# Performance work log

Measured on AMD Instinct MI355X. Metric: run time of the kernel, lower is better.

## Reference

```python
import jax, jax.numpy as jnp
import numpy as np

N = 100000
E = 1600000
IN_FEATS = 128
OUT_FEATS = 64


def setup_inputs() -> dict:
    key = jax.random.key(0)
    ks = jax.random.split(key, 8)
    node_feat = jax.random.normal(ks[0], (N, IN_FEATS), dtype=jnp.float32)
    edge_feat = jax.random.normal(ks[1], (E, 1), dtype=jnp.float32)
    # Linear params (PyTorch Linear: y = x @ W^T + b; we store W already transposed as [in, out])
    W_node = jax.random.normal(ks[2], (IN_FEATS, OUT_FEATS), dtype=jnp.float32) / np.sqrt(IN_FEATS)
    b_node = jax.random.normal(ks[3], (OUT_FEATS,), dtype=jnp.float32) * 0.01
    W_edge = jax.random.normal(ks[4], (1, OUT_FEATS), dtype=jnp.float32)
    b_edge = jax.random.normal(ks[5], (OUT_FEATS,), dtype=jnp.float32) * 0.01
    src = jax.random.randint(ks[6], (E,), 0, N, dtype=jnp.int32)
    dst = jax.random.randint(ks[7], (E,), 0, N, dtype=jnp.int32)
    return {"node_feat": node_feat, "edge_feat": edge_feat, "W_node": W_node,
            "b_node": b_node, "W_edge": W_edge, "b_edge": b_edge,
            "src": src, "dst": dst}


def reference(node_feat, edge_feat, W_node, b_node, W_edge, b_edge, src, dst):
    n_nodes = node_feat.shape[0]
    # node linear: h = node_fc(node_feat)  -> [N, out]
    h = node_feat @ W_node + b_node
    # edge linear: he = edge_fc(edge_feat) -> [E, out]
    he = edge_feat @ W_edge + b_edge
    # u_add_e: m = h[src] + he  (gather + add)  -> [E, out]
    m = h[src] + he
    # mean aggregate over destination nodes (segment mean; 0 for isolated nodes, as in DGL)
    msg_sum = jax.ops.segment_sum(m, dst, num_segments=n_nodes)  # [N, out]
    deg = jax.ops.segment_sum(jnp.ones((dst.shape[0],), dtype=m.dtype), dst, num_segments=n_nodes)  # [N]
    h_new = msg_sum / jnp.maximum(deg, 1.0)[:, None]
    return h_new
```

## Files before the change

### kernel.cpp

```cpp
#include <hip/hip_runtime.h>

#define IN_F 128
#define OUT_F 64
#define BSH 7
#define BNODES 128
#define NBMAX 800
#define MSC 6144
#define CAPB 4096

typedef __attribute__((ext_vector_type(8))) short short8;
typedef __attribute__((ext_vector_type(4))) float f32x4;

static __device__ __forceinline__ unsigned short f2bf(float f) {
    unsigned u = __float_as_uint(f);
    u += 0x7FFF + ((u >> 16) & 1);
    return (unsigned short)(u >> 16);
}

__global__ void prep_w(const float* __restrict__ W, unsigned short* __restrict__ Wt) {
    int i = blockIdx.x * 256 + threadIdx.x;
    if (i < OUT_F * IN_F) {
        int o = i >> 7, k = i & 127;
        Wt[i] = f2bf(W[k * OUT_F + o]);
    }
}

__global__ __launch_bounds__(256) void node_linear_mfma(const float* __restrict__ nf,
                                                        const unsigned short* __restrict__ Wt,
                                                        const float* __restrict__ bn,
                                                        unsigned short* __restrict__ h16,
                                                        int n_nodes, int n_tiles) {
    const int lane = threadIdx.x & 63;
    const int wid  = threadIdx.x >> 6;
    const int l15  = lane & 15;
    const int kq   = lane >> 4;

    short8 bfrag[4][4];
#pragma unroll
    for (int c = 0; c < 4; ++c)
#pragma unroll
        for (int ks = 0; ks < 4; ++ks)
            bfrag[c][ks] = *(const short8*)&Wt[(c * 16 + l15) * IN_F + ks * 32 + kq * 8];

    float bv[4];
#pragma unroll
    for (int c = 0; c < 4; ++c) bv[c] = bn[c * 16 + l15];

    for (int tile = blockIdx.x * 4 + wid; tile < n_tiles; tile += gridDim.x * 4) {
        int arow = tile * 16 + l15;
        if (arow >= n_nodes) arow = n_nodes - 1;
        const float* rp = nf + (size_t)arow * IN_F + kq * 8;

        f32x4 acc[4];
#pragma unroll
        for (int c = 0; c < 4; ++c) acc[c] = (f32x4){bv[c], bv[c], bv[c], bv[c]};

#pragma unroll
        for (int ks = 0; ks < 4; ++ks) {
            float4 x0 = *(const float4*)(rp + ks * 32);
            float4 x1 = *(const float4*)(rp + ks * 32 + 4);
            short8 af;
            af[0] = (short)f2bf(x0.x); af[1] = (short)f2bf(x0.y);
            af[2] = (short)f2bf(x0.z); af[3] = (short)f2bf(x0.w);
            af[4] = (short)f2bf(x1.x); af[5] = (short)f2bf(x1.y);
            af[6] = (short)f2bf(x1.z); af[7] = (short)f2bf(x1.w);
#pragma unroll
            for (int c = 0; c < 4; ++c)
                acc[c] = __builtin_amdgcn_mfma_f32_16x16x32_bf16(af, bfrag[c][ks], acc[c], 0, 0, 0);
        }

#pragma unroll
        for (int j = 0; j < 4; ++j) {
            int node = tile * 16 + kq * 4 + j;
            if (node < n_nodes) {
#pragma unroll
                for (int c = 0; c < 4; ++c)
                    h16[(size_t)node * OUT_F + c * 16 + l15] = f2bf(acc[c][j]);
            }
        }
    }
}

__global__ void init_cur(int* __restrict__ gcur, int nb) {
    int i = blockIdx.x * 256 + threadIdx.x;
    if (i < nb) gcur[i] = i * CAPB;
}

__global__ __launch_bounds__(512) void multisplit(const int* __restrict__ src,
                                                  const int* __restrict__ dst,
                                                  const float* __restrict__ ef,
                                                  int* __restrict__ gcur,
                                                  int2* __restrict__ es,
                                                  int n_edges, int nb) {
    __shared__ int2 stage[MSC];
    __shared__ unsigned short sbuck[MSC];
    __shared__ int lhist[NBMAX];
    __shared__ int lbase[NBMAX];
    __shared__ int lcur[NBMAX];
    __shared__ int gbase[NBMAX];
    __shared__ int part[512];

    const int t = threadIdx.x;
    const int cb = blockIdx.x * MSC;
    const int valid = min(MSC, n_edges - cb);
    if (valid <= 0) return;

    for (int i = t; i < nb; i += 512) lhist[i] = 0;
    __syncthreads();

#pragma unroll
    for (int k = 0; k < MSC / 512; ++k) {
        int i = t + (k << 9);
        if (i < valid) atomicAdd(&lhist[dst[cb + i] >> BSH], 1);
    }
    __syncthreads();

    {
        const int b0 = t * 2;
        int v0 = (b0 < nb) ? lhist[b0] : 0;
        int v1 = (b0 + 1 < nb) ? lhist[b0 + 1] : 0;
        int s = v0 + v1;
        part[t] = s;
        __syncthreads();
        for (int off = 1; off < 512; off <<= 1) {
            int x = (t >= off) ? part[t - off] : 0;
            __syncthreads();
            part[t] += x;
            __syncthreads();
        }
        int excl = part[t] - s;
        if (b0 < nb)     { lbase[b0] = excl;          lcur[b0] = excl; }
        if (b0 + 1 < nb) { lbase[b0 + 1] = excl + v0; lcur[b0 + 1] = excl + v0; }
    }
    __syncthreads();

    for (int b = t; b < nb; b += 512) {
        int c = lhist[b];
        gbase[b] = c ? atomicAdd(&gcur[b], c) : 0;
    }
    __syncthreads();

#pragma unroll
    for (int k = 0; k < MSC / 512; ++k) {
        int i = t + (k << 9);
        if (i < valid) {
            int d = dst[cb + i];
            int b = d >> BSH;
            int p = atomicAdd(&lcur[b], 1);
            int dl = d & (BNODES - 1);
            stage[p] = make_int2((dl << 17) | src[cb + i], __float_as_int(ef[cb + i]));
            sbuck[p] = (unsigned short)b;
        }
    }
    __syncthreads();

    for (int i = t; i < valid; i += 512) {
        int b = sbuck[i];
        int pos = gbase[b] + (i - lbase[b]);
        if (pos < (b + 1) * CAPB) es[pos] = stage[i];
    }
}

__global__ __launch_bounds__(512) void aggregate(const unsigned short* __restrict__ h16,
                                                 const int2* __restrict__ es,
                                                 const int* __restrict__ gcur,
                                                 const float* __restrict__ We,
                                                 const float* __restrict__ be,
                                                 float* __restrict__ out, int n_nodes) {
    __shared__ int2 stage[CAPB];
    __shared__ int lhist[BNODES];
    __shared__ int lbase[BNODES];
    __shared__ int lcur[BNODES];
    __shared__ int sc[BNODES];

    const int t = threadIdx.x;
    const int bkt = blockIdx.x;
    const int s0 = bkt * CAPB;
    int cnt = gcur[bkt] - s0;
    if (cnt > CAPB) cnt = CAPB;

    if (t < BNODES) lhist[t] = 0;
    __syncthreads();

    int2 er[8];
#pragma unroll
    for (int k = 0; k < 8; ++k) {
        int i = t + (k << 9);
        if (i < cnt) er[k] = es[s0 + i];
    }
#pragma unroll
    for (int k = 0; k < 8; ++k) {
        int i = t + (k << 9);
        if (i < cnt) atomicAdd(&lhist[((unsigned)er[k].x) >> 17], 1);
    }
    __syncthreads();

    if (t < BNODES) sc[t] = lhist[t];
    __syncthreads();
    for (int off = 1; off < BNODES; off <<= 1) {
        int v = (t < BNODES && t >= off) ? sc[t - off] : 0;
        __syncthreads();
        if (t < BNODES) sc[t] += v;
        __syncthreads();
    }
    if (t < BNODES) { int e0 = sc[t] - lhist[t]; lbase[t] = e0; lcur[t] = e0; }
    __syncthreads();

#pragma unroll
    for (int k = 0; k < 8; ++k) {
        int i = t + (k << 9);
        if (i < cnt) {
            int b = ((unsigned)er[k].x) >> 17;
            int p = atomicAdd(&lcur[b], 1);
            stage[p] = er[k];
        }
    }
    __syncthreads();

    const int wid = t >> 6;
    const int lane = t & 63;
    const int o2 = lane & 31;
    const int half = lane >> 5;
    const float2 we2 = *(const float2*)&We[o2 << 1];
    const float2 be2 = *(const float2*)&be[o2 << 1];

    for (int dl = wid; dl < BNODES; dl += 8) {
        int node = (bkt << BSH) + dl;
        if (node >= n_nodes) break;
        const int j0 = lbase[dl];
        const int dg = lhist[dl];
        float ax = 0.f, ay = 0.f, bx = 0.f, by = 0.f;
        float sx = 0.f;
        int j = 0;
        for (; j + 8 <= dg; j += 8) {
            int2 e[4];
#pragma unroll
            for (int u = 0; u < 4; ++u) e[u] = stage[j0 + j + (u << 1) + half];
            unsigned hv[4];
#pragma unroll
            for (int u = 0; u < 4; ++u)
                hv[u] = *(const unsigned*)&h16[((size_t)(e[u].x & 0x1FFFF) << 6) + (o2 << 1)];
#pragma unroll
            for (int u = 0; u < 4; ++u) {
                if (u & 1) { bx += __uint_as_float(hv[u] << 16); by += __uint_as_float(hv[u] & 0xFFFF0000u); }
                else       { ax += __uint_as_float(hv[u] << 16); ay += __uint_as_float(hv[u] & 0xFFFF0000u); }
                sx += __int_as_float(e[u].y);
            }
        }
        for (j += half; j < dg; j += 2) {
            int2 e = stage[j0 + j];
            unsigned hv = *(const unsigned*)&h16[((size_t)(e.x & 0x1FFFF) << 6) + (o2 << 1)];
            ax += __uint_as_float(hv << 16);
            ay += __uint_as_float(hv & 0xFFFF0000u);
            sx += __int_as_float(e.y);
        }
        float rx = ax + bx, ry = ay + by;
        rx += __shfl_xor(rx, 32, 64);
        ry += __shfl_xor(ry, 32, 64);
        sx += __shfl_xor(sx, 32, 64);
        if (half == 0) {
            float2 r = make_float2(0.f, 0.f);
            if (dg > 0) {
                float dgf = (float)dg;
                float inv = 1.f / dgf;
                r.x = (rx + we2.x * sx + dgf * be2.x) * inv;
                r.y = (ry + we2.y * sx + dgf * be2.y) * inv;
            }
            *(float2*)&out[((size_t)node << 6) + (o2 << 1)] = r;
        }
    }
}

extern "C" void kernel_launch(void* const* d_in, const int* in_sizes, int n_in,
                              void* d_out, int out_size, void* d_ws, size_t ws_size,
                              hipStream_t stream) {
    const float* nf  = (const float*)d_in[0];
    const float* ef  = (const float*)d_in[1];
    const float* Wn  = (const float*)d_in[2];
    const float* bn  = (const float*)d_in[3];
    const float* We  = (const float*)d_in[4];
    const float* be  = (const float*)d_in[5];
    const int*   src = (const int*)d_in[6];
    const int*   dst = (const int*)d_in[7];
    float* out = (float*)d_out;

    const int n_nodes = in_sizes[0] / IN_F;
    const int n_edges = in_sizes[6];
    const int nb = (n_nodes + BNODES - 1) >> BSH;
    const int n_tiles = (n_nodes + 15) / 16;

    char* w = (char*)d_ws;
    unsigned short* h16 = (unsigned short*)w; w += (size_t)n_nodes * OUT_F * sizeof(unsigned short);
    int2* es  = (int2*)w; w += (size_t)nb * CAPB * sizeof(int2);
    int* gcur = (int*)w;  w += (size_t)nb * sizeof(int);
    unsigned short* Wt = (unsigned short*)w; w += (size_t)OUT_F * IN_F * sizeof(unsigned short);

    init_cur<<<(nb + 255) / 256, 256, 0, stream>>>(gcur, nb);
    prep_w<<<(OUT_F * IN_F + 255) / 256, 256, 0, stream>>>(Wn, Wt);
    node_linear_mfma<<<782, 256, 0, stream>>>(nf, Wt, bn, h16, n_nodes, n_tiles);
    multisplit<<<(n_edges + MSC - 1) / MSC, 512, 0, stream>>>(src, dst, ef, gcur, es, n_edges, nb);
    aggregate<<<nb, 512, 0, stream>>>(h16, es, gcur, We, be, out, n_nodes);
}
```

Measured before the change: 92.67 us.

## Halve bucket size, cache edge loads in multisplit, and re-map aggregate lanes

Destination buckets shrink from 128 to 64 nodes, so twice as many aggregate blocks each stage half as many edges. Multisplit runs with 1024 threads and loads src, dst and ef into registers once instead of reading dst twice. Aggregate now uses 16 lanes per node with 4 features each and processes two nodes per wave at once, reducing the edge stream across 4 lane groups. The gcur init is fused into the weight-prep kernel to remove one launch. The aim is more parallelism and wider gathers in aggregate, at the cost of more global atomics and histogram work in multisplit and larger LDS use per block.

```diff
diff --git a/kernel.cpp b/kernel.cpp
--- a/kernel.cpp
+++ b/kernel.cpp
@@ -2,11 +2,11 @@
 
 #define IN_F 128
 #define OUT_F 64
-#define BSH 7
-#define BNODES 128
-#define NBMAX 800
+#define BSH 6
+#define BNODES 64
+#define NBMAX 1600
 #define MSC 6144
-#define CAPB 4096
+#define CAPB 2048
 
 typedef __attribute__((ext_vector_type(8))) short short8;
 typedef __attribute__((ext_vector_type(4))) float f32x4;
@@ -17,12 +17,14 @@
     return (unsigned short)(u >> 16);
 }
 
-__global__ void prep_w(const float* __restrict__ W, unsigned short* __restrict__ Wt) {
+__global__ void prep(const float* __restrict__ W, unsigned short* __restrict__ Wt,
+                     int* __restrict__ gcur, int nb) {
     int i = blockIdx.x * 256 + threadIdx.x;
     if (i < OUT_F * IN_F) {
         int o = i >> 7, k = i & 127;
         Wt[i] = f2bf(W[k * OUT_F + o]);
     }
+    if (i < nb) gcur[i] = i * CAPB;
 }
 
 __global__ __launch_bounds__(256) void node_linear_mfma(const float* __restrict__ nf,
@@ -81,48 +83,49 @@
     }
 }
 
-__global__ void init_cur(int* __restrict__ gcur, int nb) {
-    int i = blockIdx.x * 256 + threadIdx.x;
-    if (i < nb) gcur[i] = i * CAPB;
-}
-
-__global__ __launch_bounds__(512) void multisplit(const int* __restrict__ src,
-                                                  const int* __restrict__ dst,
-                                                  const float* __restrict__ ef,
-                                                  int* __restrict__ gcur,
-                                                  int2* __restrict__ es,
-                                                  int n_edges, int nb) {
+__global__ __launch_bounds__(1024) void multisplit(const int* __restrict__ src,
+                                                   const int* __restrict__ dst,
+                                                   const float* __restrict__ ef,
+                                                   int* __restrict__ gcur,
+                                                   int2* __restrict__ es,
+                                                   int n_edges, int nb) {
     __shared__ int2 stage[MSC];
     __shared__ unsigned short sbuck[MSC];
     __shared__ int lhist[NBMAX];
     __shared__ int lbase[NBMAX];
     __shared__ int lcur[NBMAX];
     __shared__ int gbase[NBMAX];
-    __shared__ int part[512];
+    __shared__ int part[1024];
 
     const int t = threadIdx.x;
     const int cb = blockIdx.x * MSC;
     const int valid = min(MSC, n_edges - cb);
     if (valid <= 0) return;
 
-    for (int i = t; i < nb; i += 512) lhist[i] = 0;
-    __syncthreads();
-
-#pragma unroll
-    for (int k = 0; k < MSC / 512; ++k) {
-        int i = t + (k << 9);
-        if (i < valid) atomicAdd(&lhist[dst[cb + i] >> BSH], 1);
-    }
+    for (int i = t; i < nb; i += 1024) lhist[i] = 0;
+
+    int   dr[6]; int sr[6]; float fr[6];
+#pragma unroll
+    for (int k = 0; k < 6; ++k) {
+        int i = t + (k << 10);
+        if (i < valid) { dr[k] = dst[cb + i]; sr[k] = src[cb + i]; fr[k] = ef[cb + i]; }
+        else           { dr[k] = -1; sr[k] = 0; fr[k] = 0.f; }
+    }
+    __syncthreads();
+
+#pragma unroll
+    for (int k = 0; k < 6; ++k)
+        if (dr[k] >= 0) atomicAdd(&lhist[dr[k] >> BSH], 1);
     __syncthreads();
 
     {
-        const int b0 = t * 2;
+        const int b0 = t << 1;
         int v0 = (b0 < nb) ? lhist[b0] : 0;
         int v1 = (b0 + 1 < nb) ? lhist[b0 + 1] : 0;
         int s = v0 + v1;
         part[t] = s;
         __syncthreads();
-        for (int off = 1; off < 512; off <<= 1) {
+        for (int off = 1; off < 1024; off <<= 1) {
             int x = (t >= off) ? part[t - off] : 0;
             __syncthreads();
             part[t] += x;
@@ -134,39 +137,37 @@
     }
     __syncthreads();
 
-    for (int b = t; b < nb; b += 512) {
+    for (int b = t; b < nb; b += 1024) {
         int c = lhist[b];
         gbase[b] = c ? atomicAdd(&gcur[b], c) : 0;
     }
     __syncthreads();
 
 #pragma unroll
-    for (int k = 0; k < MSC / 512; ++k) {
-        int i = t + (k << 9);
-        if (i < valid) {
-            int d = dst[cb + i];
-            int b = d >> BSH;
+    for (int k = 0; k < 6; ++k) {
+        if (dr[k] >= 0) {
+            int b = dr[k] >> BSH;
             int p = atomicAdd(&lcur[b], 1);
-            int dl = d & (BNODES - 1);
-            stage[p] = make_int2((dl << 17) | src[cb + i], __float_as_int(ef[cb + i]));
+            int dl = dr[k] & (BNODES - 1);
+            stage[p] = make_int2((dl << 17) | sr[k], __float_as_int(fr[k]));
             sbuck[p] = (unsigned short)b;
         }
     }
     __syncthreads();
 
-    for (int i = t; i < valid; i += 512) {
+    for (int i = t; i < valid; i += 1024) {
         int b = sbuck[i];
         int pos = gbase[b] + (i - lbase[b]);
         if (pos < (b + 1) * CAPB) es[pos] = stage[i];
     }
 }
 
-__global__ __launch_bounds__(512) void aggregate(const unsigned short* __restrict__ h16,
-                                                 const int2* __restrict__ es,
-                                                 const int* __restrict__ gcur,
-                                                 const float* __restrict__ We,
-                                                 const float* __restrict__ be,
-                                                 float* __restrict__ out, int n_nodes) {
+__global__ __launch_bounds__(512, 6) void aggregate(const unsigned short* __restrict__ h16,
+                                                    const int2* __restrict__ es,
+                                                    const int* __restrict__ gcur,
+                                                    const float* __restrict__ We,
+                                                    const float* __restrict__ be,
+                                                    float* __restrict__ out, int n_nodes) {
     __shared__ int2 stage[CAPB];
     __shared__ int lhist[BNODES];
     __shared__ int lbase[BNODES];
@@ -182,14 +183,14 @@
     if (t < BNODES) lhist[t] = 0;
     __syncthreads();
 
-    int2 er[8];
-#pragma unroll
-    for (int k = 0; k < 8; ++k) {
+    int2 er[4];
+#pragma unroll
+    for (int k = 0; k < 4; ++k) {
         int i = t + (k << 9);
         if (i < cnt) er[k] = es[s0 + i];
     }
 #pragma unroll
-    for (int k = 0; k < 8; ++k) {
+    for (int k = 0; k < 4; ++k) {
         int i = t + (k << 9);
         if (i < cnt) atomicAdd(&lhist[((unsigned)er[k].x) >> 17], 1);
     }
@@ -207,7 +208,7 @@
     __syncthreads();
 
 #pragma unroll
-    for (int k = 0; k < 8; ++k) {
+    for (int k = 0; k < 4; ++k) {
         int i = t + (k << 9);
         if (i < cnt) {
             int b = ((unsigned)er[k].x) >> 17;
@@ -217,56 +218,70 @@
     }
     __syncthreads();
 
-    const int wid = t >> 6;
+    const int wid  = t >> 6;
     const int lane = t & 63;
-    const int o2 = lane & 31;
-    const int half = lane >> 5;
-    const float2 we2 = *(const float2*)&We[o2 << 1];
-    const float2 be2 = *(const float2*)&be[o2 << 1];
-
-    for (int dl = wid; dl < BNODES; dl += 8) {
-        int node = (bkt << BSH) + dl;
-        if (node >= n_nodes) break;
-        const int j0 = lbase[dl];
-        const int dg = lhist[dl];
-        float ax = 0.f, ay = 0.f, bx = 0.f, by = 0.f;
-        float sx = 0.f;
-        int j = 0;
-        for (; j + 8 <= dg; j += 8) {
-            int2 e[4];
-#pragma unroll
-            for (int u = 0; u < 4; ++u) e[u] = stage[j0 + j + (u << 1) + half];
-            unsigned hv[4];
-#pragma unroll
-            for (int u = 0; u < 4; ++u)
-                hv[u] = *(const unsigned*)&h16[((size_t)(e[u].x & 0x1FFFF) << 6) + (o2 << 1)];
-#pragma unroll
-            for (int u = 0; u < 4; ++u) {
-                if (u & 1) { bx += __uint_as_float(hv[u] << 16); by += __uint_as_float(hv[u] & 0xFFFF0000u); }
-                else       { ax += __uint_as_float(hv[u] << 16); ay += __uint_as_float(hv[u] & 0xFFFF0000u); }
-                sx += __int_as_float(e[u].y);
+    const int q    = lane >> 4;
+    const int o4e  = (lane & 15) << 2;
+    const float4 we4 = *(const float4*)&We[o4e];
+    const float4 be4 = *(const float4*)&be[o4e];
+
+#pragma unroll
+    for (int p = 0; p < 4; ++p) {
+        const int dlA = (wid << 3) + (p << 1);
+        const int dlB = dlA + 1;
+        const int jA = lbase[dlA], dgA = lhist[dlA];
+        const int jB = lbase[dlB], dgB = lhist[dlB];
+        float4 aA = make_float4(0.f, 0.f, 0.f, 0.f);
+        float4 aB = make_float4(0.f, 0.f, 0.f, 0.f);
+        float sxA = 0.f, sxB = 0.f;
+        const int jm = dgA > dgB ? dgA : dgB;
+        for (int j = 0; j < jm; j += 4) {
+            int2 eA = make_int2(0, 0), eB = make_int2(0, 0);
+            if (j + q < dgA) eA = stage[jA + j + q];
+            if (j + q < dgB) eB = stage[jB + j + q];
+            uint2 hA = make_uint2(0u, 0u), hB = make_uint2(0u, 0u);
+            if (j + q < dgA) hA = *(const uint2*)&h16[((size_t)(eA.x & 0x1FFFF) << 6) + o4e];
+            if (j + q < dgB) hB = *(const uint2*)&h16[((size_t)(eB.x & 0x1FFFF) << 6) + o4e];
+            aA.x += __uint_as_float(hA.x << 16);
+            aA.y += __uint_as_float(hA.x & 0xFFFF0000u);
+            aA.z += __uint_as_float(hA.y << 16);
+            aA.w += __uint_as_float(hA.y & 0xFFFF0000u);
+            sxA  += __int_as_float(eA.y);
+            aB.x += __uint_as_float(hB.x << 16);
+            aB.y += __uint_as_float(hB.x & 0xFFFF0000u);
+            aB.z += __uint_as_float(hB.y << 16);
+            aB.w += __uint_as_float(hB.y & 0xFFFF0000u);
+            sxB  += __int_as_float(eB.y);
+        }
+#define RED_(v) { v += __shfl_xor(v, 16, 64); v += __shfl_xor(v, 32, 64); }
+        RED_(aA.x) RED_(aA.y) RED_(aA.z) RED_(aA.w) RED_(sxA)
+        RED_(aB.x) RED_(aB.y) RED_(aB.z) RED_(aB.w) RED_(sxB)
+#undef RED_
+        if (q == 0) {
+            int nodeA = (bkt << BSH) + dlA;
+            if (nodeA < n_nodes) {
+                float4 r = make_float4(0.f, 0.f, 0.f, 0.f);
+                if (dgA > 0) {
+                    float dgf = (float)dgA, inv = 1.f / dgf;
+                    r.x = (aA.x + we4.x * sxA + dgf * be4.x) * inv;
+                    r.y = (aA.y + we4.y * sxA + dgf * be4.y) * inv;
+                    r.z = (aA.z + we4.z * sxA + dgf * be4.z) * inv;
+                    r.w = (aA.w + we4.w * sxA + dgf * be4.w) * inv;
+                }
+                *(float4*)&out[((size_t)nodeA << 6) + o4e] = r;
             }
-        }
-        for (j += half; j < dg; j += 2) {
-            int2 e = stage[j0 + j];
-            unsigned hv = *(const unsigned*)&h16[((size_t)(e.x & 0x1FFFF) << 6) + (o2 << 1)];
-            ax += __uint_as_float(hv << 16);
-            ay += __uint_as_float(hv & 0xFFFF0000u);
-            sx += __int_as_float(e.y);
-        }
-        float rx = ax + bx, ry = ay + by;
-        rx += __shfl_xor(rx, 32, 64);
-        ry += __shfl_xor(ry, 32, 64);
-        sx += __shfl_xor(sx, 32, 64);
-        if (half == 0) {
-            float2 r = make_float2(0.f, 0.f);
-            if (dg > 0) {
-                float dgf = (float)dg;
-                float inv = 1.f / dgf;
-                r.x = (rx + we2.x * sx + dgf * be2.x) * inv;
-                r.y = (ry + we2.y * sx + dgf * be2.y) * inv;
+            int nodeB = (bkt << BSH) + dlB;
+            if (nodeB < n_nodes) {
+                float4 r = make_float4(0.f, 0.f, 0.f, 0.f);
+                if (dgB > 0) {
+                    float dgf = (float)dgB, inv = 1.f / dgf;
+                    r.x = (aB.x + we4.x * sxB + dgf * be4.x) * inv;
+                    r.y = (aB.y + we4.y * sxB + dgf * be4.y) * inv;
+                    r.z = (aB.z + we4.z * sxB + dgf * be4.z) * inv;
+                    r.w = (aB.w + we4.w * sxB + dgf * be4.w) * inv;
+                }
+                *(float4*)&out[((size_t)nodeB << 6) + o4e] = r;
             }
-            *(float2*)&out[((size_t)node << 6) + (o2 << 1)] = r;
         }
     }
 }
@@ -292,12 +307,11 @@
     char* w = (char*)d_ws;
     unsigned short* h16 = (unsigned short*)w; w += (size_t)n_nodes * OUT_F * sizeof(unsigned short);
     int2* es  = (int2*)w; w += (size_t)nb * CAPB * sizeof(int2);
-    int* gcur = (int*)w;  w += (size_t)nb * sizeof(int);
+    int* gcur = (int*)w;  w += (size_t)NBMAX * sizeof(int);
     unsigned short* Wt = (unsigned short*)w; w += (size_t)OUT_F * IN_F * sizeof(unsigned short);
 
-    init_cur<<<(nb + 255) / 256, 256, 0, stream>>>(gcur, nb);
-    prep_w<<<(OUT_F * IN_F + 255) / 256, 256, 0, stream>>>(Wn, Wt);
+    prep<<<32, 256, 0, stream>>>(Wn, Wt, gcur, nb);
     node_linear_mfma<<<782, 256, 0, stream>>>(nf, Wt, bn, h16, n_nodes, n_tiles);
-    multisplit<<<(n_edges + MSC - 1) / MSC, 512, 0, stream>>>(src, dst, ef, gcur, es, n_edges, nb);
+    multisplit<<<(n_edges + MSC - 1) / MSC, 1024, 0, stream>>>(src, dst, ef, gcur, es, n_edges, nb);
     aggregate<<<nb, 512, 0, stream>>>(h16, es, gcur, We, be, out, n_nodes);
 }
```

New measurement: 87.43 us. 1.06x faster.
